# Optimization experiments

Hardware: AMD Instinct MI355X
Metric: run time of the kernel (lower is better)

Reference implementation:

```python
import jax, jax.numpy as jnp
import numpy as np

N_NODES = 30000
N_EDGES = 240000
N_GRAPHS = 300
IN_CH = 5


def _bn(x, p):
    # inference batchnorm; p = stack([gamma, beta, running_mean, running_var]), shape (4, C)
    g, b, m, v = p
    return g * (x - m) * jax.lax.rsqrt(v + 1e-5) + b


def _gatv2(x, src, dst, wl, bl, wr, br, att, bias, heads, outc, concat):
    # PyG GATv2Conv: e_ij = att . leaky_relu(lin_l(x_j) + lin_r(x_i)), softmax over edges into i,
    # out_i = sum_j alpha_ij * lin_l(x_j)
    n = x.shape[0]
    xl = (x @ wl + bl).reshape(n, heads, outc)  # source-side transform
    xr = (x @ wr + br).reshape(n, heads, outc)  # target-side transform
    e = jax.nn.leaky_relu(xl[src] + xr[dst], 0.2)          # [E, H, C]
    logit = jnp.einsum('ehc,hc->eh', e, att)               # [E, H]
    lmax = jax.ops.segment_max(logit, dst, num_segments=n)
    lmax = jnp.where(jnp.isfinite(lmax), lmax, 0.0)        # empty segments -> 0
    ex = jnp.exp(logit - lmax[dst])
    den = jax.ops.segment_sum(ex, dst, num_segments=n)
    alpha = ex / (den[dst] + 1e-16)                        # PyG softmax eps
    out = jax.ops.segment_sum(xl[src] * alpha[..., None], dst, num_segments=n)
    out = out.reshape(n, heads * outc) if concat else out.mean(axis=1)
    return out + bias


def _forward(x, edge_index, batch, w_in, b_in, bn_in,
             g1_wl, g1_bl, g1_wr, g1_br, g1_att, g1_bias, bn1,
             g2_wl, g2_bl, g2_wr, g2_br, g2_att, g2_bias, bn2,
             g3_wl, g3_bl, g3_wr, g3_br, g3_att, g3_bias, bn3,
             c_w1, c_b1, c_bn, c_w2, c_b2, c_w3, c_b3):
    n = x.shape[0]
    loops = jnp.arange(n)
    src = jnp.concatenate([edge_index[0], loops])  # add_self_loops=True
    dst = jnp.concatenate([edge_index[1], loops])
    h = jax.nn.relu(_bn(x @ w_in + b_in, bn_in))
    h = jax.nn.elu(_bn(_gatv2(h, src, dst, g1_wl, g1_bl, g1_wr, g1_br, g1_att, g1_bias, 4, 64, True), bn1))
    h = jax.nn.elu(_bn(_gatv2(h, src, dst, g2_wl, g2_bl, g2_wr, g2_br, g2_att, g2_bias, 4, 64, True), bn2))
    h = jax.nn.elu(_bn(_gatv2(h, src, dst, g3_wl, g3_bl, g3_wr, g3_br, g3_att, g3_bias, 1, 128, False), bn3))
    cnt = jax.ops.segment_sum(jnp.ones((n,), h.dtype), batch, num_segments=N_GRAPHS)
    mean = jax.ops.segment_sum(h, batch, num_segments=N_GRAPHS) / jnp.maximum(cnt, 1.0)[:, None]
    mx = jax.ops.segment_max(h, batch, num_segments=N_GRAPHS)
    mx = jnp.where(jnp.isfinite(mx), mx, 0.0)
    g = jnp.concatenate([mean, mx], axis=1)                # (B, 256)
    z = jax.nn.relu(_bn(g @ c_w1 + c_b1, c_bn))
    z = jax.nn.relu(z @ c_w2 + c_b2)
    return jax.nn.log_softmax(z @ c_w3 + c_b3, axis=-1)    # (B, 2)


def setup_inputs() -> dict:
    base = jax.random.key(0)
    k = lambda i: jax.random.fold_in(base, i)
    def lin(i, fi, fo):
        return jax.random.normal(k(i), (fi, fo), jnp.float32) / np.sqrt(np.float32(fi))
    def vec(i, c):
        return jax.random.normal(k(i), (c,), jnp.float32) * 0.05
    def bn(i, c):
        g = jax.random.uniform(k(i), (c,), jnp.float32) + 0.5
        b = jax.random.normal(jax.random.fold_in(k(i), 1), (c,), jnp.float32) * 0.1
        return jnp.stack([g, b, jnp.zeros((c,), jnp.float32), jnp.ones((c,), jnp.float32)])
    def att(i, h, c):
        return jax.random.normal(k(i), (h, c), jnp.float32) / np.sqrt(np.float32(c))
    return dict(
        x=jax.random.normal(k(0), (N_NODES, IN_CH), jnp.float32),
        edge_index=jax.random.randint(k(1), (2, N_EDGES), 0, N_NODES),
        batch=jnp.sort(jax.random.randint(k(2), (N_NODES,), 0, N_GRAPHS)),
        w_in=lin(3, IN_CH, 64), b_in=vec(4, 64), bn_in=bn(5, 64),
        g1_wl=lin(6, 64, 256), g1_bl=vec(7, 256), g1_wr=lin(8, 64, 256), g1_br=vec(9, 256),
        g1_att=att(10, 4, 64), g1_bias=vec(11, 256), bn1=bn(12, 256),
        g2_wl=lin(13, 256, 256), g2_bl=vec(14, 256), g2_wr=lin(15, 256, 256), g2_br=vec(16, 256),
        g2_att=att(17, 4, 64), g2_bias=vec(18, 256), bn2=bn(19, 256),
        g3_wl=lin(20, 256, 128), g3_bl=vec(21, 128), g3_wr=lin(22, 256, 128), g3_br=vec(23, 128),
        g3_att=att(24, 1, 128), g3_bias=vec(25, 128), bn3=bn(26, 128),
        c_w1=lin(27, 256, 128), c_b1=vec(28, 128), c_bn=bn(29, 128),
        c_w2=lin(30, 128, 64), c_b2=vec(31, 64),
        c_w3=lin(32, 64, 2), c_b3=vec(33, 2),
    )


def reference(x, edge_index, batch, w_in, b_in, bn_in,
              g1_wl, g1_bl, g1_wr, g1_br, g1_att, g1_bias, bn1,
              g2_wl, g2_bl, g2_wr, g2_br, g2_att, g2_bias, bn2,
              g3_wl, g3_bl, g3_wr, g3_br, g3_att, g3_bias, bn3,
              c_w1, c_b1, c_bn, c_w2, c_b2, c_w3, c_b3):
    return _forward(x, edge_index, batch, w_in, b_in, bn_in,
                    g1_wl, g1_bl, g1_wr, g1_br, g1_att, g1_bias, bn1,
                    g2_wl, g2_bl, g2_wr, g2_br, g2_att, g2_bias, bn2,
                    g3_wl, g3_bl, g3_wr, g3_br, g3_att, g3_bias, bn3,
                    c_w1, c_b1, c_bn, c_w2, c_b2, c_w3, c_b3)
```

## Files before the change

### kernel.cpp

```cpp
#include <hip/hip_runtime.h>
#include <math.h>

#define N_NODES  30000
#define N_EDGES  240000
#define E_TOT    270000
#define N_GRAPHS 300
#define NCH      118

typedef _Float16 half8 __attribute__((ext_vector_type(8)));
typedef _Float16 half4 __attribute__((ext_vector_type(4)));
typedef _Float16 half2v __attribute__((ext_vector_type(2)));
typedef float float4v __attribute__((ext_vector_type(4)));

static inline int cdiv(int a, int b) { return (a + b - 1) / b; }

static __device__ __forceinline__ void gload_lds16(const void* g, void* l) {
    __builtin_amdgcn_global_load_lds(
        (const __attribute__((address_space(1))) void*)g,
        (__attribute__((address_space(3))) void*)l, 16, 0, 0);
}

template<int CTRL>
static __device__ __forceinline__ float ror_add(float v) {
    int t = __builtin_amdgcn_update_dpp(0, __float_as_int(v), CTRL, 0xF, 0xF, false);
    return v + __int_as_float(t);
}
static __device__ __forceinline__ float red16(float v) {
    v = ror_add<0x128>(v);
    v = ror_add<0x124>(v);
    v = ror_add<0x122>(v);
    v = ror_add<0x121>(v);
    return v;
}

__device__ inline void wp_dev(const float* __restrict__ W, _Float16* __restrict__ Wt,
                              int K, int CO, int gtid, int T) {
    int tot = K * CO;
    for (int i = gtid; i < tot; i += T) {
        int k = i / CO, c = i - k * CO;
        Wt[(size_t)c * K + k] = (_Float16)W[i];
    }
}

__global__ void hist_wprep_input(const int* __restrict__ ei, int* __restrict__ deg,
                                 const float* __restrict__ x, const float* __restrict__ w_in,
                                 const float* __restrict__ b_in, const float* __restrict__ bn_in,
                                 _Float16* __restrict__ a16,
                                 const float* __restrict__ w1l, const float* __restrict__ w1r,
                                 const float* __restrict__ w2l, const float* __restrict__ w2r,
                                 const float* __restrict__ w3l, const float* __restrict__ w3r,
                                 _Float16* __restrict__ t1l, _Float16* __restrict__ t1r,
                                 _Float16* __restrict__ t2l, _Float16* __restrict__ t2r,
                                 _Float16* __restrict__ t3l, _Float16* __restrict__ t3r) {
    int gtid = blockIdx.x * blockDim.x + threadIdx.x;
    int T = gridDim.x * blockDim.x;
    for (int e = gtid; e < E_TOT; e += T) {
        int d = (e < N_EDGES) ? ei[N_EDGES + e] : e - N_EDGES;
        atomicAdd(&deg[d], 1);
    }
    wp_dev(w1l, t1l, 64, 256, gtid, T);
    wp_dev(w1r, t1r, 64, 256, gtid, T);
    wp_dev(w2l, t2l, 256, 256, gtid, T);
    wp_dev(w2r, t2r, 256, 256, gtid, T);
    wp_dev(w3l, t3l, 256, 128, gtid, T);
    wp_dev(w3r, t3r, 256, 128, gtid, T);

    int lane = threadIdx.x & 63;
    int wv = blockIdx.x * (blockDim.x >> 6) + (threadIdx.x >> 6);
    int NW = gridDim.x * (blockDim.x >> 6);
    float g = bn_in[lane], be = bn_in[64 + lane];
    float m = bn_in[128 + lane], va = bn_in[192 + lane];
    float rs = rsqrtf(va + 1e-5f);
    float wcol[5];
#pragma unroll
    for (int ci = 0; ci < 5; ++ci) wcol[ci] = w_in[ci * 64 + lane];
    float bb = b_in[lane];
    for (int n = wv; n < N_NODES; n += NW) {
        float xv = (lane < 5) ? x[n * 5 + lane] : 0.f;
        float acc = bb;
#pragma unroll
        for (int ci = 0; ci < 5; ++ci)
            acc = fmaf(__shfl(xv, ci, 64), wcol[ci], acc);
        acc = g * (acc - m) * rs + be;
        a16[(size_t)n * 64 + lane] = (_Float16)fmaxf(acc, 0.f);
    }
}

__global__ __launch_bounds__(256)
void scan_all(const int* __restrict__ deg, const int* __restrict__ batch,
              int* __restrict__ row_start, int* __restrict__ gstart) {
    __shared__ int red[256];
    __shared__ int s[256];
    const int b = blockIdx.x, t = threadIdx.x;
    int pre = 0;
    for (int i = t; i < b * 256; i += 256) pre += deg[i];
    red[t] = pre;
    __syncthreads();
    for (int off = 128; off; off >>= 1) {
        if (t < off) red[t] += red[t + off];
        __syncthreads();
    }
    int base = red[0];
    int gid = b * 256 + t;
    int v = (gid < N_NODES) ? deg[gid] : 0;
    s[t] = v;
    __syncthreads();
    for (int off = 1; off < 256; off <<= 1) {
        int u = (t >= off) ? s[t - off] : 0;
        __syncthreads();
        s[t] += u;
        __syncthreads();
    }
    if (gid < N_NODES) row_start[gid] = base + s[t] - v;
    if (b == 0 && t == 0) row_start[N_NODES] = E_TOT;
    if (b == 0) {
        for (int g = t; g <= N_GRAPHS; g += 256) {
            int lo = 0, hi = N_NODES;
            while (lo < hi) {
                int mid = (lo + hi) >> 1;
                if (batch[mid] < g) lo = mid + 1;
                else                hi = mid;
            }
            gstart[g] = lo;
        }
    }
}

template<int K, int COUT, int SCAT>
__global__ __launch_bounds__(256, 4)
void gemm_mfma(const _Float16* __restrict__ A,
               const _Float16* __restrict__ Wtl, const float* __restrict__ bl,
               const _Float16* __restrict__ Wtr, const float* __restrict__ br,
               _Float16* __restrict__ outl, _Float16* __restrict__ outr,
               const int* __restrict__ ei, const int* __restrict__ row_start,
               int* __restrict__ cnt, int* __restrict__ esrc, int N) {
    constexpr int BM = 128, BN = 128, BK = 64;
    constexpr int CSL = COUT / BN > 0 ? COUT / BN : 1;
    if (SCAT && blockIdx.y == 2 * CSL) {
        int gtid = blockIdx.x * blockDim.x + threadIdx.x;
        int T = gridDim.x * blockDim.x;
        for (int e = gtid; e < E_TOT; e += T) {
            int s, d;
            if (e < N_EDGES) { s = ei[e]; d = ei[N_EDGES + e]; }
            else             { s = e - N_EDGES; d = s; }
            int slot = row_start[d] + atomicAdd(&cnt[d], 1);
            esrc[slot] = s;
        }
        return;
    }
    __shared__ __attribute__((aligned(16))) _Float16 As[BM * BK];
    __shared__ __attribute__((aligned(16))) _Float16 Bs[BN * BK];
    const int tid  = threadIdx.x;
    const int wave = tid >> 6;
    const int lane = tid & 63;
    const int l15  = lane & 15;
    const int lq   = lane >> 4;
    const int n0   = blockIdx.x * BM;
    const int sel  = blockIdx.y / CSL;
    const int col0 = (blockIdx.y % CSL) * BN;
    const _Float16* Wt = sel ? Wtr : Wtl;
    const float* bias  = sel ? br : bl;
    _Float16* out      = sel ? outr : outl;

    const int r0 = tid >> 3;
    const int us = (tid & 7) ^ (r0 & 7);

    float4v acc[2][8];
#pragma unroll
    for (int mi = 0; mi < 2; ++mi)
#pragma unroll
        for (int nt = 0; nt < 8; ++nt)
#pragma unroll
            for (int r = 0; r < 4; ++r) acc[mi][nt][r] = 0.f;

    for (int kt = 0; kt < K; kt += BK) {
#pragma unroll
        for (int p = 0; p < 4; ++p) {
            int row = p * 32 + r0;
            int gn  = n0 + row;
            if (gn >= N) gn = 0;
            gload_lds16(A + (size_t)gn * K + kt + us * 8, As + (p * 256 + tid) * 8);
        }
#pragma unroll
        for (int p = 0; p < 4; ++p) {
            int row = p * 32 + r0;
            gload_lds16(Wt + (size_t)(col0 + row) * K + kt + us * 8, Bs + (p * 256 + tid) * 8);
        }
        __syncthreads();
#pragma unroll
        for (int kk = 0; kk < BK; kk += 32) {
            const int sw = (lq + (kk >> 3)) ^ (l15 & 7);
            half8 af0 = *(const half8*)(As + (wave * 32 + l15) * BK + sw * 8);
            half8 af1 = *(const half8*)(As + (wave * 32 + 16 + l15) * BK + sw * 8);
#pragma unroll
            for (int nt = 0; nt < 8; ++nt) {
                half8 bf = *(const half8*)(Bs + (nt * 16 + l15) * BK + sw * 8);
                acc[0][nt] = __builtin_amdgcn_mfma_f32_16x16x32_f16(af0, bf, acc[0][nt], 0, 0, 0);
                acc[1][nt] = __builtin_amdgcn_mfma_f32_16x16x32_f16(af1, bf, acc[1][nt], 0, 0, 0);
            }
        }
        __syncthreads();
    }
#pragma unroll
    for (int mi = 0; mi < 2; ++mi)
#pragma unroll
        for (int nt = 0; nt < 8; ++nt) {
            int col = col0 + nt * 16 + l15;
            float bv = bias[col];
#pragma unroll
            for (int r = 0; r < 4; ++r) {
                int row = n0 + wave * 32 + mi * 16 + lq * 4 + r;
                if (row < N)
                    out[(size_t)row * COUT + col] = (_Float16)(acc[mi][nt][r] + bv);
            }
        }
}

template<typename TOUT>
__global__ __launch_bounds__(256)
void gat_gather4(const _Float16* __restrict__ xl, const _Float16* __restrict__ xr,
                 const int* __restrict__ row_start, const int* __restrict__ esrc,
                 const float* __restrict__ att, const float* __restrict__ gbias,
                 const float* __restrict__ bnp, TOUT* __restrict__ out) {
    constexpr int HC = 256, PER = 4;
    int node = (blockIdx.x * blockDim.x + threadIdx.x) >> 6;
    int lane = threadIdx.x & 63;
    if (node >= N_NODES) return;
    const int base = lane * PER;

    float rr[PER], av[PER], acc[PER];
    {
        half4 rv = *(const half4*)(xr + (size_t)node * HC + base);
#pragma unroll
        for (int k = 0; k < PER; ++k) rr[k] = (float)rv[k];
        *(float4*)av = *(const float4*)(att + base);
    }
#pragma unroll
    for (int k = 0; k < PER; ++k) acc[k] = 0.f;

    float l = 0.f;
    const int j0 = row_start[node], j1 = row_start[node + 1];
    for (int jc = j0; jc < j1; jc += 64) {
        int nedge = min(64, j1 - jc);
        int ev = (jc + lane < j1) ? esrc[jc + lane] : 0;
        for (int jj = 0; jj < nedge; jj += 4) {
            int s[4];
            bool val[4];
#pragma unroll
            for (int u = 0; u < 4; ++u) {
                int idx = jj + u;
                val[u] = idx < nedge;
                s[u] = __shfl(ev, val[u] ? idx : jj, 64);
            }
            float xs[4][PER];
#pragma unroll
            for (int u = 0; u < 4; ++u) {
                half4 xv = *(const half4*)(xl + (size_t)s[u] * HC + base);
#pragma unroll
                for (int k = 0; k < PER; ++k) xs[u][k] = (float)xv[k];
            }
            float pz[4];
#pragma unroll
            for (int u = 0; u < 4; ++u) {
                float pp = 0.f;
#pragma unroll
                for (int k = 0; k < PER; ++k) {
                    float v = xs[u][k] + rr[k];
                    v = (v > 0.f) ? v : 0.2f * v;
                    pp = fmaf(v, av[k], pp);
                }
                pz[u] = red16(pp);
            }
            float w[4];
#pragma unroll
            for (int u = 0; u < 4; ++u) w[u] = val[u] ? __expf(pz[u]) : 0.f;
            l += (w[0] + w[1]) + (w[2] + w[3]);
#pragma unroll
            for (int k = 0; k < PER; ++k)
                acc[k] += fmaf(w[0], xs[0][k],
                          fmaf(w[1], xs[1][k],
                          fmaf(w[2], xs[2][k], w[3] * xs[3][k])));
        }
    }
    float inv = 1.f / (l + 1e-16f);
    float o[PER];
#pragma unroll
    for (int k = 0; k < PER; ++k) {
        float v = fmaf(acc[k], inv, gbias[base + k]);
        float g  = bnp[base + k], be = bnp[HC + base + k];
        float mm = bnp[2 * HC + base + k], va = bnp[3 * HC + base + k];
        v = g * (v - mm) * rsqrtf(va + 1e-5f) + be;
        o[k] = (v > 0.f) ? v : (__expf(v) - 1.f);
    }
    half4 ov;
#pragma unroll
    for (int k = 0; k < PER; ++k) ov[k] = (_Float16)o[k];
    *(half4*)((_Float16*)out + (size_t)node * HC + base) = ov;
}

__global__ __launch_bounds__(256)
void gat_gather1(const _Float16* __restrict__ xl, const _Float16* __restrict__ xr,
                 const int* __restrict__ row_start, const int* __restrict__ esrc,
                 const float* __restrict__ att, const float* __restrict__ gbias,
                 const float* __restrict__ bnp, float* __restrict__ out) {
    constexpr int HC = 128, PER = 4;
    int node = (blockIdx.x * blockDim.x + threadIdx.x) >> 6;
    int lane = threadIdx.x & 63;
    if (node >= N_NODES) return;
    const int half = lane >> 5;
    const int base = (lane & 31) * PER;

    float rr[PER], av[PER], acc[PER];
    {
        half4 rv = *(const half4*)(xr + (size_t)node * HC + base);
#pragma unroll
        for (int k = 0; k < PER; ++k) rr[k] = (float)rv[k];
        *(float4*)av = *(const float4*)(att + base);
    }
#pragma unroll
    for (int k = 0; k < PER; ++k) acc[k] = 0.f;

    float l = 0.f;
    const int j0 = row_start[node], j1 = row_start[node + 1];
    for (int jc = j0; jc < j1; jc += 64) {
        int nedge = min(64, j1 - jc);
        int ev = (jc + lane < j1) ? esrc[jc + lane] : 0;
        for (int jj = 0; jj < nedge; jj += 8) {
            int s[4];
            bool val[4];
#pragma unroll
            for (int u = 0; u < 4; ++u) {
                int idx = jj + 2 * u + half;
                val[u] = idx < nedge;
                s[u] = __shfl(ev, val[u] ? idx : jj, 64);
            }
            float xs[4][PER];
#pragma unroll
            for (int u = 0; u < 4; ++u) {
                half4 xv = *(const half4*)(xl + (size_t)s[u] * HC + base);
#pragma unroll
                for (int k = 0; k < PER; ++k) xs[u][k] = (float)xv[k];
            }
            float pz[4];
#pragma unroll
            for (int u = 0; u < 4; ++u) {
                float pp = 0.f;
#pragma unroll
                for (int k = 0; k < PER; ++k) {
                    float v = xs[u][k] + rr[k];
                    v = (v > 0.f) ? v : 0.2f * v;
                    pp = fmaf(v, av[k], pp);
                }
                pp += __shfl_xor(pp, 16, 64);
                pz[u] = red16(pp);
            }
            float w[4];
#pragma unroll
            for (int u = 0; u < 4; ++u) w[u] = val[u] ? __expf(pz[u]) : 0.f;
            l += (w[0] + w[1]) + (w[2] + w[3]);
#pragma unroll
            for (int k = 0; k < PER; ++k)
                acc[k] += fmaf(w[0], xs[0][k],
                          fmaf(w[1], xs[1][k],
                          fmaf(w[2], xs[2][k], w[3] * xs[3][k])));
        }
    }
    l += __shfl_xor(l, 32, 64);
#pragma unroll
    for (int k = 0; k < PER; ++k) acc[k] += __shfl_xor(acc[k], 32, 64);

    if (half == 0) {
        float inv = 1.f / (l + 1e-16f);
        float o[PER];
#pragma unroll
        for (int k = 0; k < PER; ++k) {
            float v = fmaf(acc[k], inv, gbias[base + k]);
            float g  = bnp[base + k], be = bnp[HC + base + k];
            float mm = bnp[2 * HC + base + k], va = bnp[3 * HC + base + k];
            v = g * (v - mm) * rsqrtf(va + 1e-5f) + be;
            o[k] = (v > 0.f) ? v : (__expf(v) - 1.f);
        }
        *(float4*)(out + (size_t)node * HC + base) = *(float4*)o;
    }
}

__global__ __launch_bounds__(512)
void pool_cls(const float* __restrict__ h, const int* __restrict__ gstart,
              const float* __restrict__ w1, const float* __restrict__ b1,
              const float* __restrict__ bnp,
              const float* __restrict__ w2, const float* __restrict__ b2,
              const float* __restrict__ w3, const float* __restrict__ b3,
              float* __restrict__ out) {
    __shared__ float part[512];
    __shared__ float sg[256];
    __shared__ float sz1[128];
    __shared__ float sz2[64];
    __shared__ float sz3[2];
    int g = blockIdx.x, t = threadIdx.x;
    int c = t & 127, q = t >> 7;
    int a = gstart[g], b = gstart[g + 1];
    float sum = 0.f, mx = -INFINITY;
    for (int i = a + q; i < b; i += 4) {
        float v = h[(size_t)i * 128 + c];
        sum += v;
        mx = fmaxf(mx, v);
    }
    part[t] = sum;
    __syncthreads();
    if (q == 0)
        sg[c] = (part[c] + part[c + 128] + part[c + 256] + part[c + 384])
                / fmaxf((float)(b - a), 1.f);
    __syncthreads();
    part[t] = mx;
    __syncthreads();
    if (q == 0) {
        float m2 = fmaxf(fmaxf(part[c], part[c + 128]),
                         fmaxf(part[c + 256], part[c + 384]));
        sg[128 + c] = (b > a) ? m2 : 0.f;
    }
    __syncthreads();
    float acc = 0.f;
    for (int i = q * 64; i < q * 64 + 64; ++i) acc += sg[i] * w1[i * 128 + c];
    part[t] = acc;
    __syncthreads();
    if (q == 0) {
        float z = part[c] + part[c + 128] + part[c + 256] + part[c + 384] + b1[c];
        float ga = bnp[c], be = bnp[128 + c], m = bnp[256 + c], va = bnp[384 + c];
        z = ga * (z - m) * rsqrtf(va + 1e-5f) + be;
        sz1[c] = fmaxf(z, 0.f);
    }
    __syncthreads();
    if (t < 128) {
        int o = t & 63, q2 = t >> 6;
        float a2 = 0.f;
        for (int i = q2 * 64; i < q2 * 64 + 64; ++i) a2 += sz1[i] * w2[i * 64 + o];
        part[t] = a2;
    }
    __syncthreads();
    if (t < 64) sz2[t] = fmaxf(part[t] + part[t + 64] + b2[t], 0.f);
    __syncthreads();
    if (t < 2) {
        float a3 = b3[t];
        for (int i = 0; i < 64; ++i) a3 += sz2[i] * w3[i * 2 + t];
        sz3[t] = a3;
    }
    __syncthreads();
    if (t < 2) {
        float mm = fmaxf(sz3[0], sz3[1]);
        float lse = mm + logf(expf(sz3[0] - mm) + expf(sz3[1] - mm));
        out[g * 2 + t] = sz3[t] - lse;
    }
}

extern "C" void kernel_launch(void* const* d_in, const int* in_sizes, int n_in,
                              void* d_out, int out_size, void* d_ws, size_t ws_size,
                              hipStream_t stream) {
    const float* x       = (const float*)d_in[0];
    const int*   ei      = (const int*)d_in[1];
    const int*   batch   = (const int*)d_in[2];
    const float* w_in    = (const float*)d_in[3];
    const float* b_in    = (const float*)d_in[4];
    const float* bn_in   = (const float*)d_in[5];
    const float* g1_wl   = (const float*)d_in[6];
    const float* g1_bl   = (const float*)d_in[7];
    const float* g1_wr   = (const float*)d_in[8];
    const float* g1_br   = (const float*)d_in[9];
    const float* g1_att  = (const float*)d_in[10];
    const float* g1_bias = (const float*)d_in[11];
    const float* bn1     = (const float*)d_in[12];
    const float* g2_wl   = (const float*)d_in[13];
    const float* g2_bl   = (const float*)d_in[14];
    const float* g2_wr   = (const float*)d_in[15];
    const float* g2_br   = (const float*)d_in[16];
    const float* g2_att  = (const float*)d_in[17];
    const float* g2_bias = (const float*)d_in[18];
    const float* bn2     = (const float*)d_in[19];
    const float* g3_wl   = (const float*)d_in[20];
    const float* g3_bl   = (const float*)d_in[21];
    const float* g3_wr   = (const float*)d_in[22];
    const float* g3_br   = (const float*)d_in[23];
    const float* g3_att  = (const float*)d_in[24];
    const float* g3_bias = (const float*)d_in[25];
    const float* bn3     = (const float*)d_in[26];
    const float* c_w1    = (const float*)d_in[27];
    const float* c_b1    = (const float*)d_in[28];
    const float* c_bn    = (const float*)d_in[29];
    const float* c_w2    = (const float*)d_in[30];
    const float* c_b2    = (const float*)d_in[31];
    const float* c_w3    = (const float*)d_in[32];
    const float* c_b3    = (const float*)d_in[33];
    float* out = (float*)d_out;

    const size_t NHC = (size_t)N_NODES * 256;
    _Float16* a16  = (_Float16*)d_ws;
    _Float16* xl16 = a16 + NHC;
    _Float16* xr16 = xl16 + NHC;
    _Float16* wt = xr16 + NHC;
    _Float16* wt1l = wt;            _Float16* wt1r = wt + 16384;
    _Float16* wt2l = wt + 32768;    _Float16* wt2r = wt + 98304;
    _Float16* wt3l = wt + 163840;   _Float16* wt3r = wt + 196608;
    float* fbase = (float*)(wt + 262144);
    float* bufD = fbase;
    int* iw = (int*)(bufD + (size_t)N_NODES * 128);
    int* deg       = iw;            int* cnt    = iw + 30000;
    int* row_start = iw + 90128;
    int* esrc      = iw + 120129;
    int* gstart    = iw + 390429;

    const int BT = 256;
    const int NT128 = cdiv(N_NODES, 128);

    hipMemsetAsync(deg, 0, 60000 * sizeof(int), stream);

    hist_wprep_input<<<1024, BT, 0, stream>>>(ei, deg, x, w_in, b_in, bn_in, a16,
                                              g1_wl, g1_wr, g2_wl, g2_wr, g3_wl, g3_wr,
                                              wt1l, wt1r, wt2l, wt2r, wt3l, wt3r);
    scan_all<<<NCH, 256, 0, stream>>>(deg, batch, row_start, gstart);

    gemm_mfma<64, 256, 1><<<dim3(NT128, 5), 256, 0, stream>>>(
        a16, wt1l, g1_bl, wt1r, g1_br, xl16, xr16, ei, row_start, cnt, esrc, N_NODES);
    gat_gather4<_Float16><<<cdiv(N_NODES * 64, BT), BT, 0, stream>>>(
        xl16, xr16, row_start, esrc, g1_att, g1_bias, bn1, a16);

    gemm_mfma<256, 256, 0><<<dim3(NT128, 4), 256, 0, stream>>>(
        a16, wt2l, g2_bl, wt2r, g2_br, xl16, xr16, nullptr, nullptr, nullptr, nullptr, N_NODES);
    gat_gather4<_Float16><<<cdiv(N_NODES * 64, BT), BT, 0, stream>>>(
        xl16, xr16, row_start, esrc, g2_att, g2_bias, bn2, a16);

    gemm_mfma<256, 128, 0><<<dim3(NT128, 2), 256, 0, stream>>>(
        a16, wt3l, g3_bl, wt3r, g3_br, xl16, xr16, nullptr, nullptr, nullptr, nullptr, N_NODES);
    gat_gather1<<<cdiv(N_NODES * 64, BT), BT, 0, stream>>>(
        xl16, xr16, row_start, esrc, g3_att, g3_bias, bn3, bufD);

    pool_cls<<<N_GRAPHS, 512, 0, stream>>>(bufD, gstart, c_w1, c_b1, c_bn,
                                           c_w2, c_b2, c_w3, c_b3, out);
}
```

Baseline: 315.6 us.

## Remap GEMM blocks per XCD, vectorize epilogue stores, widen gather lanes

The GEMM now runs on a 1D grid and remaps block IDs so that consecutive tiles land on the same XCD, which should improve L2 reuse of the A tiles. Its MFMA operands are swapped so each lane holds four consecutive columns, letting the epilogue write half4 vectors instead of scalar halves. The gather kernels now load eight halves per lane: the 4-head kernel splits a wave into two halves that work on different edges, and the single-head kernel splits it into four. This halves or quarters the cross-lane reduction width and raises memory-level parallelism, at the cost of extra shuffle reductions at the end and more registers.

Measured after the change: 345.9 us. +9.6%, slower.

```diff
diff --git a/kernel.cpp b/kernel.cpp
--- a/kernel.cpp
+++ b/kernel.cpp
@@ -9,7 +9,6 @@
 
 typedef _Float16 half8 __attribute__((ext_vector_type(8)));
 typedef _Float16 half4 __attribute__((ext_vector_type(4)));
-typedef _Float16 half2v __attribute__((ext_vector_type(2)));
 typedef float float4v __attribute__((ext_vector_type(4)));
 
 static inline int cdiv(int a, int b) { return (a + b - 1) / b; }
@@ -21,15 +20,21 @@
 }
 
 template<int CTRL>
-static __device__ __forceinline__ float ror_add(float v) {
+static __device__ __forceinline__ float dpp_add(float v) {
     int t = __builtin_amdgcn_update_dpp(0, __float_as_int(v), CTRL, 0xF, 0xF, false);
     return v + __int_as_float(t);
 }
 static __device__ __forceinline__ float red16(float v) {
-    v = ror_add<0x128>(v);
-    v = ror_add<0x124>(v);
-    v = ror_add<0x122>(v);
-    v = ror_add<0x121>(v);
+    v = dpp_add<0x128>(v);
+    v = dpp_add<0x124>(v);
+    v = dpp_add<0x122>(v);
+    v = dpp_add<0x121>(v);
+    return v;
+}
+static __device__ __forceinline__ float red8(float v) {
+    v = dpp_add<0x141>(v);
+    v = dpp_add<0xB1>(v);
+    v = dpp_add<0x4E>(v);
     return v;
 }
 
@@ -136,9 +141,13 @@
                int* __restrict__ cnt, int* __restrict__ esrc, int N) {
     constexpr int BM = 128, BN = 128, BK = 64;
     constexpr int CSL = COUT / BN > 0 ? COUT / BN : 1;
-    if (SCAT && blockIdx.y == 2 * CSL) {
-        int gtid = blockIdx.x * blockDim.x + threadIdx.x;
-        int T = gridDim.x * blockDim.x;
+    constexpr int NS  = 2 * CSL;
+    const int NT  = (N + BM - 1) / BM;
+    const int nwg = NT * NS;
+    const int id  = blockIdx.x;
+    if (SCAT && id >= nwg) {
+        int gtid = (id - nwg) * blockDim.x + threadIdx.x;
+        int T = (gridDim.x - nwg) * blockDim.x;
         for (int e = gtid; e < E_TOT; e += T) {
             int s, d;
             if (e < N_EDGES) { s = ei[e]; d = ei[N_EDGES + e]; }
@@ -148,6 +157,10 @@
         }
         return;
     }
+    const int q = nwg >> 3, r = nwg & 7, xcd = id & 7, kk_ = id >> 3;
+    const int rm = (xcd < r ? xcd * (q + 1) : r * (q + 1) + (xcd - r) * q) + kk_;
+    const int tile = rm / NS, slice = rm % NS;
+
     __shared__ __attribute__((aligned(16))) _Float16 As[BM * BK];
     __shared__ __attribute__((aligned(16))) _Float16 Bs[BN * BK];
     const int tid  = threadIdx.x;
@@ -155,9 +168,9 @@
     const int lane = tid & 63;
     const int l15  = lane & 15;
     const int lq   = lane >> 4;
-    const int n0   = blockIdx.x * BM;
-    const int sel  = blockIdx.y / CSL;
-    const int col0 = (blockIdx.y % CSL) * BN;
+    const int n0   = tile * BM;
+    const int sel  = slice / CSL;
+    const int col0 = (slice % CSL) * BN;
     const _Float16* Wt = sel ? Wtr : Wtl;
     const float* bias  = sel ? br : bl;
     _Float16* out      = sel ? outr : outl;
@@ -171,7 +184,7 @@
 #pragma unroll
         for (int nt = 0; nt < 8; ++nt)
 #pragma unroll
-            for (int r = 0; r < 4; ++r) acc[mi][nt][r] = 0.f;
+            for (int r2 = 0; r2 < 4; ++r2) acc[mi][nt][r2] = 0.f;
 
     for (int kt = 0; kt < K; kt += BK) {
 #pragma unroll
@@ -195,25 +208,28 @@
 #pragma unroll
             for (int nt = 0; nt < 8; ++nt) {
                 half8 bf = *(const half8*)(Bs + (nt * 16 + l15) * BK + sw * 8);
-                acc[0][nt] = __builtin_amdgcn_mfma_f32_16x16x32_f16(af0, bf, acc[0][nt], 0, 0, 0);
-                acc[1][nt] = __builtin_amdgcn_mfma_f32_16x16x32_f16(af1, bf, acc[1][nt], 0, 0, 0);
+                acc[0][nt] = __builtin_amdgcn_mfma_f32_16x16x32_f16(bf, af0, acc[0][nt], 0, 0, 0);
+                acc[1][nt] = __builtin_amdgcn_mfma_f32_16x16x32_f16(bf, af1, acc[1][nt], 0, 0, 0);
             }
         }
         __syncthreads();
     }
 #pragma unroll
-    for (int mi = 0; mi < 2; ++mi)
-#pragma unroll
-        for (int nt = 0; nt < 8; ++nt) {
-            int col = col0 + nt * 16 + l15;
-            float bv = bias[col];
-#pragma unroll
-            for (int r = 0; r < 4; ++r) {
-                int row = n0 + wave * 32 + mi * 16 + lq * 4 + r;
-                if (row < N)
-                    out[(size_t)row * COUT + col] = (_Float16)(acc[mi][nt][r] + bv);
-            }
-        }
+    for (int mi = 0; mi < 2; ++mi) {
+        int row = n0 + wave * 32 + mi * 16 + l15;
+        if (row < N) {
+#pragma unroll
+            for (int nt = 0; nt < 8; ++nt) {
+                int col = col0 + nt * 16 + lq * 4;
+                float4v bv = *(const float4v*)(bias + col);
+                half4 hv;
+#pragma unroll
+                for (int r2 = 0; r2 < 4; ++r2)
+                    hv[r2] = (_Float16)(acc[mi][nt][r2] + bv[r2]);
+                *(half4*)(out + (size_t)row * COUT + col) = hv;
+            }
+        }
+    }
 }
 
 template<typename TOUT>
@@ -222,88 +238,7 @@
                  const int* __restrict__ row_start, const int* __restrict__ esrc,
                  const float* __restrict__ att, const float* __restrict__ gbias,
                  const float* __restrict__ bnp, TOUT* __restrict__ out) {
-    constexpr int HC = 256, PER = 4;
-    int node = (blockIdx.x * blockDim.x + threadIdx.x) >> 6;
-    int lane = threadIdx.x & 63;
-    if (node >= N_NODES) return;
-    const int base = lane * PER;
-
-    float rr[PER], av[PER], acc[PER];
-    {
-        half4 rv = *(const half4*)(xr + (size_t)node * HC + base);
-#pragma unroll
-        for (int k = 0; k < PER; ++k) rr[k] = (float)rv[k];
-        *(float4*)av = *(const float4*)(att + base);
-    }
-#pragma unroll
-    for (int k = 0; k < PER; ++k) acc[k] = 0.f;
-
-    float l = 0.f;
-    const int j0 = row_start[node], j1 = row_start[node + 1];
-    for (int jc = j0; jc < j1; jc += 64) {
-        int nedge = min(64, j1 - jc);
-        int ev = (jc + lane < j1) ? esrc[jc + lane] : 0;
-        for (int jj = 0; jj < nedge; jj += 4) {
-            int s[4];
-            bool val[4];
-#pragma unroll
-            for (int u = 0; u < 4; ++u) {
-                int idx = jj + u;
-                val[u] = idx < nedge;
-                s[u] = __shfl(ev, val[u] ? idx : jj, 64);
-            }
-            float xs[4][PER];
-#pragma unroll
-            for (int u = 0; u < 4; ++u) {
-                half4 xv = *(const half4*)(xl + (size_t)s[u] * HC + base);
-#pragma unroll
-                for (int k = 0; k < PER; ++k) xs[u][k] = (float)xv[k];
-            }
-            float pz[4];
-#pragma unroll
-            for (int u = 0; u < 4; ++u) {
-                float pp = 0.f;
-#pragma unroll
-                for (int k = 0; k < PER; ++k) {
-                    float v = xs[u][k] + rr[k];
-                    v = (v > 0.f) ? v : 0.2f * v;
-                    pp = fmaf(v, av[k], pp);
-                }
-                pz[u] = red16(pp);
-            }
-            float w[4];
-#pragma unroll
-            for (int u = 0; u < 4; ++u) w[u] = val[u] ? __expf(pz[u]) : 0.f;
-            l += (w[0] + w[1]) + (w[2] + w[3]);
-#pragma unroll
-            for (int k = 0; k < PER; ++k)
-                acc[k] += fmaf(w[0], xs[0][k],
-                          fmaf(w[1], xs[1][k],
-                          fmaf(w[2], xs[2][k], w[3] * xs[3][k])));
-        }
-    }
-    float inv = 1.f / (l + 1e-16f);
-    float o[PER];
-#pragma unroll
-    for (int k = 0; k < PER; ++k) {
-        float v = fmaf(acc[k], inv, gbias[base + k]);
-        float g  = bnp[base + k], be = bnp[HC + base + k];
-        float mm = bnp[2 * HC + base + k], va = bnp[3 * HC + base + k];
-        v = g * (v - mm) * rsqrtf(va + 1e-5f) + be;
-        o[k] = (v > 0.f) ? v : (__expf(v) - 1.f);
-    }
-    half4 ov;
-#pragma unroll
-    for (int k = 0; k < PER; ++k) ov[k] = (_Float16)o[k];
-    *(half4*)((_Float16*)out + (size_t)node * HC + base) = ov;
-}
-
-__global__ __launch_bounds__(256)
-void gat_gather1(const _Float16* __restrict__ xl, const _Float16* __restrict__ xr,
-                 const int* __restrict__ row_start, const int* __restrict__ esrc,
-                 const float* __restrict__ att, const float* __restrict__ gbias,
-                 const float* __restrict__ bnp, float* __restrict__ out) {
-    constexpr int HC = 128, PER = 4;
+    constexpr int HC = 256, PER = 8;
     int node = (blockIdx.x * blockDim.x + threadIdx.x) >> 6;
     int lane = threadIdx.x & 63;
     if (node >= N_NODES) return;
@@ -312,10 +247,11 @@
 
     float rr[PER], av[PER], acc[PER];
     {
-        half4 rv = *(const half4*)(xr + (size_t)node * HC + base);
+        half8 rv = *(const half8*)(xr + (size_t)node * HC + base);
 #pragma unroll
         for (int k = 0; k < PER; ++k) rr[k] = (float)rv[k];
-        *(float4*)av = *(const float4*)(att + base);
+        *(float4v*)av       = *(const float4v*)(att + base);
+        *(float4v*)(av + 4) = *(const float4v*)(att + base + 4);
     }
 #pragma unroll
     for (int k = 0; k < PER; ++k) acc[k] = 0.f;
@@ -337,7 +273,7 @@
             float xs[4][PER];
 #pragma unroll
             for (int u = 0; u < 4; ++u) {
-                half4 xv = *(const half4*)(xl + (size_t)s[u] * HC + base);
+                half8 xv = *(const half8*)(xl + (size_t)s[u] * HC + base);
 #pragma unroll
                 for (int k = 0; k < PER; ++k) xs[u][k] = (float)xv[k];
             }
@@ -351,8 +287,7 @@
                     v = (v > 0.f) ? v : 0.2f * v;
                     pp = fmaf(v, av[k], pp);
                 }
-                pp += __shfl_xor(pp, 16, 64);
-                pz[u] = red16(pp);
+                pz[u] = red8(pp);
             }
             float w[4];
 #pragma unroll
@@ -370,6 +305,97 @@
     for (int k = 0; k < PER; ++k) acc[k] += __shfl_xor(acc[k], 32, 64);
 
     if (half == 0) {
+        float inv = 1.f / (l + 1e-16f);
+        half8 ov;
+#pragma unroll
+        for (int k = 0; k < PER; ++k) {
+            float v = fmaf(acc[k], inv, gbias[base + k]);
+            float g  = bnp[base + k], be = bnp[HC + base + k];
+            float mm = bnp[2 * HC + base + k], va = bnp[3 * HC + base + k];
+            v = g * (v - mm) * rsqrtf(va + 1e-5f) + be;
+            v = (v > 0.f) ? v : (__expf(v) - 1.f);
+            ov[k] = (_Float16)v;
+        }
+        *(half8*)((_Float16*)out + (size_t)node * HC + base) = ov;
+    }
+}
+
+__global__ __launch_bounds__(256)
+void gat_gather1(const _Float16* __restrict__ xl, const _Float16* __restrict__ xr,
+                 const int* __restrict__ row_start, const int* __restrict__ esrc,
+                 const float* __restrict__ att, const float* __restrict__ gbias,
+                 const float* __restrict__ bnp, float* __restrict__ out) {
+    constexpr int HC = 128, PER = 8;
+    int node = (blockIdx.x * blockDim.x + threadIdx.x) >> 6;
+    int lane = threadIdx.x & 63;
+    if (node >= N_NODES) return;
+    const int qt   = lane >> 4;
+    const int base = (lane & 15) * PER;
+
+    float rr[PER], av[PER], acc[PER];
+    {
+        half8 rv = *(const half8*)(xr + (size_t)node * HC + base);
+#pragma unroll
+        for (int k = 0; k < PER; ++k) rr[k] = (float)rv[k];
+        *(float4v*)av       = *(const float4v*)(att + base);
+        *(float4v*)(av + 4) = *(const float4v*)(att + base + 4);
+    }
+#pragma unroll
+    for (int k = 0; k < PER; ++k) acc[k] = 0.f;
+
+    float l = 0.f;
+    const int j0 = row_start[node], j1 = row_start[node + 1];
+    for (int jc = j0; jc < j1; jc += 64) {
+        int nedge = min(64, j1 - jc);
+        int ev = (jc + lane < j1) ? esrc[jc + lane] : 0;
+        for (int jj = 0; jj < nedge; jj += 16) {
+            int s[4];
+            bool val[4];
+#pragma unroll
+            for (int u = 0; u < 4; ++u) {
+                int idx = jj + 4 * u + qt;
+                val[u] = idx < nedge;
+                s[u] = __shfl(ev, val[u] ? idx : jj, 64);
+            }
+            float xs[4][PER];
+#pragma unroll
+            for (int u = 0; u < 4; ++u) {
+                half8 xv = *(const half8*)(xl + (size_t)s[u] * HC + base);
+#pragma unroll
+                for (int k = 0; k < PER; ++k) xs[u][k] = (float)xv[k];
+            }
+            float pz[4];
+#pragma unroll
+            for (int u = 0; u < 4; ++u) {
+                float pp = 0.f;
+#pragma unroll
+                for (int k = 0; k < PER; ++k) {
+                    float v = xs[u][k] + rr[k];
+                    v = (v > 0.f) ? v : 0.2f * v;
+                    pp = fmaf(v, av[k], pp);
+                }
+                pz[u] = red16(pp);
+            }
+            float w[4];
+#pragma unroll
+            for (int u = 0; u < 4; ++u) w[u] = val[u] ? __expf(pz[u]) : 0.f;
+            l += (w[0] + w[1]) + (w[2] + w[3]);
+#pragma unroll
+            for (int k = 0; k < PER; ++k)
+                acc[k] += fmaf(w[0], xs[0][k],
+                          fmaf(w[1], xs[1][k],
+                          fmaf(w[2], xs[2][k], w[3] * xs[3][k])));
+        }
+    }
+    l += __shfl_xor(l, 16, 64);
+    l += __shfl_xor(l, 32, 64);
+#pragma unroll
+    for (int k = 0; k < PER; ++k) {
+        acc[k] += __shfl_xor(acc[k], 16, 64);
+        acc[k] += __shfl_xor(acc[k], 32, 64);
+    }
+
+    if (qt == 0) {
         float inv = 1.f / (l + 1e-16f);
         float o[PER];
 #pragma unroll
@@ -380,7 +406,8 @@
             v = g * (v - mm) * rsqrtf(va + 1e-5f) + be;
             o[k] = (v > 0.f) ? v : (__expf(v) - 1.f);
         }
-        *(float4*)(out + (size_t)node * HC + base) = *(float4*)o;
+        *(float4v*)(out + (size_t)node * HC + base)     = *(float4v*)o;
+        *(float4v*)(out + (size_t)node * HC + base + 4) = *(float4v*)(o + 4);
     }
 }
 
@@ -517,17 +544,17 @@
                                               wt1l, wt1r, wt2l, wt2r, wt3l, wt3r);
     scan_all<<<NCH, 256, 0, stream>>>(deg, batch, row_start, gstart);
 
-    gemm_mfma<64, 256, 1><<<dim3(NT128, 5), 256, 0, stream>>>(
+    gemm_mfma<64, 256, 1><<<NT128 * 4 + NT128, 256, 0, stream>>>(
         a16, wt1l, g1_bl, wt1r, g1_br, xl16, xr16, ei, row_start, cnt, esrc, N_NODES);
     gat_gather4<_Float16><<<cdiv(N_NODES * 64, BT), BT, 0, stream>>>(
         xl16, xr16, row_start, esrc, g1_att, g1_bias, bn1, a16);
 
-    gemm_mfma<256, 256, 0><<<dim3(NT128, 4), 256, 0, stream>>>(
+    gemm_mfma<256, 256, 0><<<NT128 * 4, 256, 0, stream>>>(
         a16, wt2l, g2_bl, wt2r, g2_br, xl16, xr16, nullptr, nullptr, nullptr, nullptr, N_NODES);
     gat_gather4<_Float16><<<cdiv(N_NODES * 64, BT), BT, 0, stream>>>(
         xl16, xr16, row_start, esrc, g2_att, g2_bias, bn2, a16);
 
-    gemm_mfma<256, 128, 0><<<dim3(NT128, 2), 256, 0, stream>>>(
+    gemm_mfma<256, 128, 0><<<NT128 * 2, 256, 0, stream>>>(
         a16, wt3l, g3_bl, wt3r, g3_br, xl16, xr16, nullptr, nullptr, nullptr, nullptr, N_NODES);
     gat_gather1<<<cdiv(N_NODES * 64, BT), BT, 0, stream>>>(
         xl16, xr16, row_start, esrc, g3_att, g3_bias, bn3, bufD);
```
